# Optimization experiments

Hardware: AMD Instinct MI355X
Metric: run time of the kernel (lower is better)

## Reference

```python
import jax, jax.numpy as jnp
import numpy as np

D_MODEL = 256
D_STATE = 16
D_CONV = 3
D_INNER = 256          # expand=1
D_HALF = D_INNER // 2  # 128
DT_RANK = 16           # ceil(256/16)
B, L0, L1 = 4, 4096, 4096


def setup_inputs() -> dict:
    key = jax.random.key(0)
    ks = jax.random.split(key, 10)
    u_0 = jax.random.normal(ks[0], (B, L0, D_MODEL), jnp.float32)
    u_1 = jax.random.normal(ks[1], (B, L1, D_MODEL), jnp.float32)
    in_proj_w = jax.random.normal(ks[2], (D_INNER, D_MODEL), jnp.float32) * (D_MODEL ** -0.5)
    conv_x_w = jax.random.normal(ks[3], (D_HALF, 1, D_CONV), jnp.float32) * (D_CONV ** -0.5)
    conv_z_w = jax.random.normal(ks[4], (D_HALF, 1, D_CONV), jnp.float32) * (D_CONV ** -0.5)
    x_proj_w = jax.random.normal(ks[5], (DT_RANK + 2 * D_STATE, D_HALF), jnp.float32) * (D_HALF ** -0.5)
    dt_init_std = DT_RANK ** -0.5
    dt_proj_w = jax.random.uniform(ks[6], (D_HALF, DT_RANK), jnp.float32, -dt_init_std, dt_init_std)
    # dt bias = inverse-softplus of dt ~ LogUniform(1e-3, 1e-1)
    dt = jnp.exp(jax.random.uniform(ks[7], (D_HALF,), jnp.float32) * (np.log(0.1) - np.log(0.001)) + np.log(0.001))
    dt = jnp.clip(dt, 1e-4, None)
    dt_proj_b = dt + jnp.log(-jnp.expm1(-dt))
    A_log = jnp.log(jnp.broadcast_to(jnp.arange(1, D_STATE + 1, dtype=jnp.float32), (D_HALF, D_STATE)))
    D_param = jnp.ones((D_HALF,), jnp.float32)
    out_proj_w = jax.random.normal(ks[8], (D_MODEL, D_INNER), jnp.float32) * (D_INNER ** -0.5)
    return {"u_0": u_0, "u_1": u_1, "in_proj_w": in_proj_w, "conv_x_w": conv_x_w,
            "conv_z_w": conv_z_w, "x_proj_w": x_proj_w, "dt_proj_w": dt_proj_w,
            "dt_proj_b": dt_proj_b, "A_log": A_log, "D": D_param, "out_proj_w": out_proj_w}


def _dwconv(x, w):
    # x: [B, C, L], w: [C, 1, K] depthwise, padding='same', no bias (conv_bias//2 == 0)
    return jax.lax.conv_general_dilated(
        x, w, window_strides=(1,), padding='SAME',
        feature_group_count=x.shape[1], dimension_numbers=('NCH', 'OIH', 'NCH'))


def _selective_scan(u, delta, A, Bm, Cm, Dv):
    # u, delta: [B, L, d]; A: [d, n]; Bm, Cm: [B, L, n]; Dv: [d]
    dA = jnp.exp(delta[..., None] * A)                       # [B, L, d, n]
    dBu = (delta * u)[..., None] * Bm[:, :, None, :]         # [B, L, d, n]
    def combine(c1, c2):
        a1, b1 = c1
        a2, b2 = c2
        return a2 * a1, a2 * b1 + b2
    _, h = jax.lax.associative_scan(combine, (dA, dBu), axis=1)  # h: [B, L, d, n]
    return jnp.einsum('bldn,bln->bld', h, Cm) + u * Dv


def _stream(u, in_proj_w, conv_x_w, conv_z_w, x_proj_w, dt_proj_w, dt_proj_b, A, D, out_proj_w):
    xz = jnp.einsum('bld,ed->ble', u, in_proj_w)             # [B, L, d_inner]
    x, z = jnp.split(xz, 2, axis=-1)                         # [B, L, d_half] each
    x = jnp.swapaxes(x, 1, 2)                                # [B, d_half, L]
    z = jnp.swapaxes(z, 1, 2)
    x_f = jax.nn.silu(_dwconv(x, conv_x_w))
    z_f = jax.nn.silu(_dwconv(z, conv_z_w))
    xf = jnp.swapaxes(x_f, 1, 2)                             # [B, L, d_half]
    dbl = jnp.einsum('bld,ed->ble', xf, x_proj_w)            # [B, L, dt_rank + 2n]
    dt, Bm, Cm = jnp.split(dbl, [DT_RANK, DT_RANK + D_STATE], axis=-1)
    dt = jnp.einsum('blr,dr->bld', dt, dt_proj_w)
    delta = jax.nn.softplus(dt + dt_proj_b)                  # delta_bias + delta_softplus
    y = _selective_scan(xf, delta, A, Bm, Cm, D)             # [B, L, d_half]
    cat = jnp.concatenate([y, jnp.swapaxes(z_f, 1, 2)], axis=-1)  # [B, L, d_inner]
    return jnp.einsum('ble,oe->blo', cat, out_proj_w)


def reference(u_0, u_1, in_proj_w, conv_x_w, conv_z_w, x_proj_w, dt_proj_w, dt_proj_b, A_log, D, out_proj_w):
    A = -jnp.exp(A_log)
    out0 = _stream(u_0, in_proj_w, conv_x_w, conv_z_w, x_proj_w, dt_proj_w, dt_proj_b, A, D, out_proj_w)
    out1 = _stream(u_1, in_proj_w, conv_x_w, conv_z_w, x_proj_w, dt_proj_w, dt_proj_b, A, D, out_proj_w)
    return (out0, out1)
```

## Files before the change

kernel.cpp:

```cpp
#include <hip/hip_runtime.h>
#include <hip/hip_bf16.h>
#include <cstdint>

#define DEV __device__ __forceinline__

typedef __attribute__((ext_vector_type(8))) short short8;
typedef __attribute__((ext_vector_type(4))) float f32x4;
typedef __attribute__((ext_vector_type(4))) unsigned short us4;
typedef __attribute__((ext_vector_type(8))) unsigned short us8;

DEV unsigned short f2bf(float x) {
    unsigned int u = __float_as_uint(x);
    unsigned int r = (u + 0x7FFFu + ((u >> 16) & 1u)) >> 16;
    return (unsigned short)r;
}
DEV float bf2f(unsigned short h) { return __uint_as_float(((unsigned int)h) << 16); }

DEV void gld_lds16(const unsigned short* g, unsigned short* l) {
    __builtin_amdgcn_global_load_lds(
        (const __attribute__((address_space(1))) unsigned int*)g,
        (__attribute__((address_space(3))) unsigned int*)l, 16, 0, 0);
}

#define LL 4096
#define DM 256
#define DH 128
#define SB_TOT 8
#define CH1 32
#define NCH 128
#define LOG2E 1.44269504088896f

__global__ __launch_bounds__(256) void prep_kernel(
    const float* __restrict__ u0, const float* __restrict__ u1,
    const float* __restrict__ inw, const float* __restrict__ outw,
    const float* __restrict__ xpw, const float* __restrict__ dtw,
    unsigned short* __restrict__ ubf, unsigned short* __restrict__ wbi,
    unsigned short* __restrict__ wbo, unsigned short* __restrict__ Wb)
{
    int gid = blockIdx.x * 256 + threadIdx.x;
    int i = gid * 4;
    if (i < 4194304) {
        f32x4 v = *(const f32x4*)&u0[i];
        us4 r = { f2bf(v.x), f2bf(v.y), f2bf(v.z), f2bf(v.w) };
        *(us4*)&ubf[i] = r;
    } else if (i < 8388608) {
        int j = i - 4194304;
        f32x4 v = *(const f32x4*)&u1[j];
        us4 r = { f2bf(v.x), f2bf(v.y), f2bf(v.z), f2bf(v.w) };
        *(us4*)&ubf[4194304 + j] = r;
    } else if (i < 8454144) {
        int j = i - 8388608;
        f32x4 v = *(const f32x4*)&inw[j];
        us4 r = { f2bf(v.x), f2bf(v.y), f2bf(v.z), f2bf(v.w) };
        *(us4*)&wbi[j] = r;
    } else if (i < 8519680) {
        int j = i - 8454144;
        f32x4 v = *(const f32x4*)&outw[j];
        us4 r = { f2bf(v.x), f2bf(v.y), f2bf(v.z), f2bf(v.w) };
        *(us4*)&wbo[j] = r;
    } else if (i < 8540160) {
        int j = i - 8519680;
        int n = j >> 7, k0 = j & 127;
        if (n < 128) {
            float a0 = 0.f, a1 = 0.f, a2 = 0.f, a3 = 0.f;
            const float* dw = dtw + n * 16;
            #pragma unroll
            for (int r = 0; r < 16; ++r) {
                float w = dw[r];
                const float* xr = xpw + r * 128 + k0;
                a0 = fmaf(w, xr[0], a0);
                a1 = fmaf(w, xr[1], a1);
                a2 = fmaf(w, xr[2], a2);
                a3 = fmaf(w, xr[3], a3);
            }
            us4 rr = { f2bf(a0), f2bf(a1), f2bf(a2), f2bf(a3) };
            *(us4*)&Wb[n * 128 + k0] = rr;
        } else {
            f32x4 v = *(const f32x4*)&xpw[(n - 112) * 128 + k0];
            us4 rr = { f2bf(v.x), f2bf(v.y), f2bf(v.z), f2bf(v.w) };
            *(us4*)&Wb[n * 128 + k0] = rr;
        }
    }
}

template<int F32OUT>
__global__ __launch_bounds__(256) void gemm_bt(
    const unsigned short* __restrict__ A, const unsigned short* __restrict__ B,
    float* __restrict__ Cf, unsigned short* __restrict__ Cb)
{
    __shared__ __align__(16) unsigned short As[128 * 32];
    __shared__ __align__(16) unsigned short Bs[128 * 32];
    const int t = threadIdx.x;
    const int m0 = blockIdx.x * 128, n0 = blockIdx.y * 128;
    const int lane = t & 63, wv = t >> 6;
    const int wm = (wv & 1) * 64, wn = (wv >> 1) * 64;
    const int lr = lane & 15, lk = (lane >> 4) * 8;
    const int srow = lane >> 2, scol = (lane & 3) * 8;

    f32x4 acc[4][4] = {};
    for (int kt = 0; kt < 8; ++kt) {
        const int k0 = kt * 32;
        #pragma unroll
        for (int h = 0; h < 2; ++h) {
            const int c = wv + h * 4;
            const unsigned short* ga = A + (size_t)(m0 + c * 16 + srow) * 256 + k0 + scol;
            const unsigned short* gb = B + (size_t)(n0 + c * 16 + srow) * 256 + k0 + scol;
            gld_lds16(ga, &As[c * 512]);
            gld_lds16(gb, &Bs[c * 512]);
        }
        __syncthreads();
        short8 av[4], bv[4];
        #pragma unroll
        for (int i = 0; i < 4; ++i) av[i] = *(const short8*)&As[(wm + i * 16 + lr) * 32 + lk];
        #pragma unroll
        for (int i = 0; i < 4; ++i) bv[i] = *(const short8*)&Bs[(wn + i * 16 + lr) * 32 + lk];
        #pragma unroll
        for (int i = 0; i < 4; ++i)
            #pragma unroll
            for (int j = 0; j < 4; ++j)
                acc[i][j] = __builtin_amdgcn_mfma_f32_16x16x32_bf16(av[i], bv[j], acc[i][j], 0, 0, 0);
        __syncthreads();
    }
    #pragma unroll
    for (int i = 0; i < 4; ++i) {
        #pragma unroll
        for (int j = 0; j < 4; ++j) {
            int r0 = m0 + wm + i * 16 + (lane >> 4) * 4;
            int cc = n0 + wn + j * 16 + lr;
            #pragma unroll
            for (int r = 0; r < 4; ++r) {
                float v = acc[i][j][r];
                if (F32OUT) Cf[(size_t)(r0 + r) * 256 + cc] = v;
                else        Cb[(size_t)(r0 + r) * 256 + cc] = f2bf(v);
            }
        }
    }
}

template<int FUSE_SCAN>
__global__ __launch_bounds__(256) void convproj_k(
    const unsigned short* __restrict__ xz, const unsigned short* __restrict__ Wb,
    const float* __restrict__ wx, const float* __restrict__ wz,
    const float* __restrict__ dtb, const float* __restrict__ alog,
    float* __restrict__ xf, unsigned short* __restrict__ catb,
    float* __restrict__ delta, float* __restrict__ BC,
    float* __restrict__ P, float* __restrict__ H)
{
    __shared__ __align__(16) char smem[35840];
    unsigned short* As = (unsigned short*)smem;
    float* dl_s = (float*)smem;
    float* xf_s = (float*)(smem + 16896);
    float* bc_s = (float*)(smem + 33792);
    const int t = threadIdx.x;
    const int kk = blockIdx.x & 7, yy = blockIdx.x >> 3;
    const int m0 = (4 * kk + (yy & 3) + 32 * (yy >> 2)) * 32;

    #pragma unroll
    for (int i = 0; i < 4; ++i) {
        int s = t + i * 256;
        int r = s >> 5, g = s & 31;
        int gr = m0 + r;
        int l = gr & 4095;
        int c; const float* wp; const unsigned short* bp;
        if (g < 16) { c = g * 8;        wp = wx; bp = xz + (size_t)gr * 256 + c; }
        else        { c = (g - 16) * 8; wp = wz; bp = xz + (size_t)gr * 256 + 128 + c; }
        us8 zz = (us8)0;
        us8 vm = (l > 0)    ? *(const us8*)(bp - 256) : zz;
        us8 v0 = *(const us8*)bp;
        us8 vp = (l < 4095) ? *(const us8*)(bp + 256) : zz;
        float o[8];
        #pragma unroll
        for (int j = 0; j < 8; ++j) {
            int cc = c + j;
            float v = bf2f(vm[j]) * wp[cc * 3] + bf2f(v0[j]) * wp[cc * 3 + 1]
                    + bf2f(vp[j]) * wp[cc * 3 + 2];
            v = v / (1.f + __expf(-v));
            o[j] = v;
        }
        us8 rb8 = { f2bf(o[0]), f2bf(o[1]), f2bf(o[2]), f2bf(o[3]),
                    f2bf(o[4]), f2bf(o[5]), f2bf(o[6]), f2bf(o[7]) };
        if (g < 16) {
            *(us8*)&As[r * 136 + c] = rb8;
            *(f32x4*)&xf_s[r * 132 + c]     = *(f32x4*)&o[0];
            *(f32x4*)&xf_s[r * 132 + c + 4] = *(f32x4*)&o[4];
            *(f32x4*)&xf[(size_t)gr * 128 + c]     = *(f32x4*)&o[0];
            *(f32x4*)&xf[(size_t)gr * 128 + c + 4] = *(f32x4*)&o[4];
        } else {
            *(us8*)&catb[(size_t)gr * 256 + 128 + c] = rb8;
        }
    }
    __syncthreads();
    const int lane = t & 63, wv = t >> 6;
    const int lr = lane & 15, lk = (lane >> 4) * 8;
    const int rt = (wv & 1) * 16;
    const int jbase = (wv >> 1) * 5;
    f32x4 acc[5] = {};
    #pragma unroll
    for (int kt = 0; kt < 4; ++kt) {
        const int k0 = kt * 32;
        short8 av = *(const short8*)&As[(rt + lr) * 136 + k0 + lk];
        #pragma unroll
        for (int j = 0; j < 5; ++j) {
            short8 bv = *(const short8*)(Wb + ((jbase + j) * 16 + lr) * 128 + k0 + lk);
            acc[j] = __builtin_amdgcn_mfma_f32_16x16x32_bf16(av, bv, acc[j], 0, 0, 0);
        }
    }
    __syncthreads();
    const int r0 = (lane >> 4) * 4;
    #pragma unroll
    for (int j = 0; j < 5; ++j) {
        int jj = jbase + j;
        int col = jj * 16 + lr;
        #pragma unroll
        for (int r = 0; r < 4; ++r) {
            float v = acc[j][r];
            int lrow = rt + r0 + r;
            size_t row = (size_t)m0 + lrow;
            if (jj < 8) {
                float x = v + dtb[col];
                float sp = (x > 20.f) ? x : __logf(1.f + __expf(x));
                delta[row * 128 + col] = sp;
                if (FUSE_SCAN) dl_s[lrow * 132 + col] = sp;
            } else {
                BC[row * 32 + (col - 128)] = v;
                if (FUSE_SCAN && jj == 8) bc_s[lrow * 16 + lr] = v;
            }
        }
    }
    if (!FUSE_SCAN) return;

    __syncthreads();
    const int hh = t >> 7, tl = t & 127;
    const int sb = m0 >> 12;
    const int ch = (m0 & 4095) >> 5;
    float Ar[8];
    #pragma unroll
    for (int n = 0; n < 8; ++n) Ar[n] = -__expf(alog[tl * 16 + hh * 8 + n]) * LOG2E;
    float h[8], p[8];
    #pragma unroll
    for (int n = 0; n < 8; ++n) { h[n] = 0.f; p[n] = 1.f; }
    #pragma unroll 4
    for (int i = 0; i < CH1; ++i) {
        float dt = dl_s[i * 132 + tl];
        float du = dt * xf_s[i * 132 + tl];
        float bl[8];
        *(f32x4*)&bl[0] = *(const f32x4*)&bc_s[i * 16 + hh * 8];
        *(f32x4*)&bl[4] = *(const f32x4*)&bc_s[i * 16 + hh * 8 + 4];
        #pragma unroll
        for (int n = 0; n < 8; ++n) {
            float a = exp2f(dt * Ar[n]);
            h[n] = fmaf(a, h[n], du * bl[n]);
            p[n] *= a;
        }
    }
    size_t ob = (((size_t)sb * NCH + ch) * 128 + tl) * 16 + hh * 8;
    f32x4 pv0 = { p[0], p[1], p[2], p[3] };
    f32x4 pv1 = { p[4], p[5], p[6], p[7] };
    f32x4 hv0 = { h[0], h[1], h[2], h[3] };
    f32x4 hv1 = { h[4], h[5], h[6], h[7] };
    *(f32x4*)&P[ob]     = pv0;
    *(f32x4*)&P[ob + 4] = pv1;
    *(f32x4*)&H[ob]     = hv0;
    *(f32x4*)&H[ob + 4] = hv1;
}

__global__ __launch_bounds__(128) void scan_p1(
    const float* __restrict__ delta, const float* __restrict__ xf,
    const float* __restrict__ BC, const float* __restrict__ alog,
    float* __restrict__ P, float* __restrict__ H)
{
    __shared__ float b_s[CH1 * 16];
    int t = threadIdx.x;
    int ch = blockIdx.x, sb = blockIdx.y;
    size_t rb = (size_t)sb * LL + (size_t)ch * CH1;
    {
        int row = t >> 2, c4 = (t & 3) * 4;
        *(f32x4*)&b_s[row * 16 + c4] = *(const f32x4*)&BC[(rb + row) * 32 + c4];
    }
    __syncthreads();
    float Ar[16];
    #pragma unroll
    for (int n = 0; n < 16; ++n) Ar[n] = -__expf(alog[t * 16 + n]) * LOG2E;
    float dtr[32], ur[32];
    #pragma unroll
    for (int i = 0; i < 32; ++i) dtr[i] = delta[(rb + i) * DH + t];
    #pragma unroll
    for (int i = 0; i < 32; ++i) ur[i] = xf[(rb + i) * DH + t];
    float h[16], p[16];
    #pragma unroll
    for (int n = 0; n < 16; ++n) { h[n] = 0.f; p[n] = 1.f; }
    for (int i = 0; i < CH1; ++i) {
        float dt = dtr[i];
        float du = dt * ur[i];
        float bl[16];
        *(f32x4*)&bl[0]  = *(const f32x4*)&b_s[i * 16];
        *(f32x4*)&bl[4]  = *(const f32x4*)&b_s[i * 16 + 4];
        *(f32x4*)&bl[8]  = *(const f32x4*)&b_s[i * 16 + 8];
        *(f32x4*)&bl[12] = *(const f32x4*)&b_s[i * 16 + 12];
        #pragma unroll
        for (int n = 0; n < 16; ++n) {
            float a = exp2f(dt * Ar[n]);
            h[n] = fmaf(a, h[n], du * bl[n]);
            p[n] *= a;
        }
    }
    size_t ob = (((size_t)sb * NCH + ch) * 128 + t) * 16;
    #pragma unroll
    for (int n4 = 0; n4 < 16; n4 += 4) {
        f32x4 pv = { p[n4], p[n4 + 1], p[n4 + 2], p[n4 + 3] };
        f32x4 hv = { h[n4], h[n4 + 1], h[n4 + 2], h[n4 + 3] };
        *(f32x4*)&P[ob + n4] = pv;
        *(f32x4*)&H[ob + n4] = hv;
    }
}

__global__ __launch_bounds__(256) void scan_p2(const float* __restrict__ P, float* __restrict__ H)
{
    __shared__ float Ps[NCH * 16], Hs[NCH * 16];
    int t = threadIdx.x;
    int d = blockIdx.x, sb = blockIdx.y;
    for (int q = t; q < NCH * 4; q += 256) {
        int ch = q >> 2, c4 = (q & 3) * 4;
        size_t g = (((size_t)sb * NCH + ch) * 128 + d) * 16 + c4;
        *(f32x4*)&Ps[ch * 16 + c4] = *(const f32x4*)&P[g];
        *(f32x4*)&Hs[ch * 16 + c4] = *(const f32x4*)&H[g];
    }
    __syncthreads();
    if (t < 16) {
        float hin = 0.f;
        for (int c = 0; c < NCH; ++c) {
            float pp = Ps[c * 16 + t], hl = Hs[c * 16 + t];
            Hs[c * 16 + t] = hin;
            hin = fmaf(pp, hin, hl);
        }
    }
    __syncthreads();
    for (int q = t; q < NCH * 4; q += 256) {
        int ch = q >> 2, c4 = (q & 3) * 4;
        size_t g = (((size_t)sb * NCH + ch) * 128 + d) * 16 + c4;
        *(f32x4*)&H[g] = *(const f32x4*)&Hs[ch * 16 + c4];
    }
}

__global__ __launch_bounds__(128) void scan_p3(
    const float* __restrict__ delta, const float* __restrict__ xf,
    const float* __restrict__ BC, const float* __restrict__ alog,
    const float* __restrict__ Dp, const float* __restrict__ H,
    unsigned short* __restrict__ catb)
{
    __shared__ float b_s[CH1 * 16];
    __shared__ float c_s[CH1 * 16];
    int t = threadIdx.x;
    int ch = blockIdx.x, sb = blockIdx.y;
    size_t rb = (size_t)sb * LL + (size_t)ch * CH1;
    {
        int row = t >> 2, c4 = (t & 3) * 4;
        *(f32x4*)&b_s[row * 16 + c4] = *(const f32x4*)&BC[(rb + row) * 32 + c4];
        *(f32x4*)&c_s[row * 16 + c4] = *(const f32x4*)&BC[(rb + row) * 32 + 16 + c4];
    }
    __syncthreads();
    float Ar[16];
    #pragma unroll
    for (int n = 0; n < 16; ++n) Ar[n] = -__expf(alog[t * 16 + n]) * LOG2E;
    float Dv = Dp[t];
    float dtr[32], ur[32];
    #pragma unroll
    for (int i = 0; i < 32; ++i) dtr[i] = delta[(rb + i) * DH + t];
    #pragma unroll
    for (int i = 0; i < 32; ++i) ur[i] = xf[(rb + i) * DH + t];
    size_t ob = (((size_t)sb * NCH + ch) * 128 + t) * 16;
    float h[16];
    #pragma unroll
    for (int n4 = 0; n4 < 16; n4 += 4) {
        f32x4 hv = *(const f32x4*)&H[ob + n4];
        h[n4] = hv.x; h[n4 + 1] = hv.y; h[n4 + 2] = hv.z; h[n4 + 3] = hv.w;
    }
    for (int i = 0; i < CH1; ++i) {
        float dt = dtr[i];
        float uu = ur[i];
        float du = dt * uu;
        float bl[16], cl[16];
        *(f32x4*)&bl[0]  = *(const f32x4*)&b_s[i * 16];
        *(f32x4*)&bl[4]  = *(const f32x4*)&b_s[i * 16 + 4];
        *(f32x4*)&bl[8]  = *(const f32x4*)&b_s[i * 16 + 8];
        *(f32x4*)&bl[12] = *(const f32x4*)&b_s[i * 16 + 12];
        *(f32x4*)&cl[0]  = *(const f32x4*)&c_s[i * 16];
        *(f32x4*)&cl[4]  = *(const f32x4*)&c_s[i * 16 + 4];
        *(f32x4*)&cl[8]  = *(const f32x4*)&c_s[i * 16 + 8];
        *(f32x4*)&cl[12] = *(const f32x4*)&c_s[i * 16 + 12];
        float y0 = uu * Dv, y1 = 0.f, y2 = 0.f, y3 = 0.f;
        #pragma unroll
        for (int n = 0; n < 16; n += 4) {
            float a0 = exp2f(dt * Ar[n]);
            float a1 = exp2f(dt * Ar[n + 1]);
            float a2 = exp2f(dt * Ar[n + 2]);
            float a3 = exp2f(dt * Ar[n + 3]);
            h[n]     = fmaf(a0, h[n],     du * bl[n]);
            h[n + 1] = fmaf(a1, h[n + 1], du * bl[n + 1]);
            h[n + 2] = fmaf(a2, h[n + 2], du * bl[n + 2]);
            h[n + 3] = fmaf(a3, h[n + 3], du * bl[n + 3]);
            y0 = fmaf(h[n],     cl[n],     y0);
            y1 = fmaf(h[n + 1], cl[n + 1], y1);
            y2 = fmaf(h[n + 2], cl[n + 2], y2);
            y3 = fmaf(h[n + 3], cl[n + 3], y3);
        }
        float y = (y0 + y1) + (y2 + y3);
        catb[(rb + i) * DM + t] = f2bf(y);
    }
}

extern "C" void kernel_launch(void* const* d_in, const int* in_sizes, int n_in,
                              void* d_out, int out_size, void* d_ws, size_t ws_size,
                              hipStream_t stream) {
    const float* u0   = (const float*)d_in[0];
    const float* u1   = (const float*)d_in[1];
    const float* inw  = (const float*)d_in[2];
    const float* cxw  = (const float*)d_in[3];
    const float* czw  = (const float*)d_in[4];
    const float* xpw  = (const float*)d_in[5];
    const float* dtw  = (const float*)d_in[6];
    const float* dtb  = (const float*)d_in[7];
    const float* alog = (const float*)d_in[8];
    const float* Dp   = (const float*)d_in[9];
    const float* outw = (const float*)d_in[10];

    char* ws = (char*)d_ws;
    unsigned short* ubf  = (unsigned short*)(ws + 0);
    float* delta         = (float*)(ws + 0);
    unsigned short* xzbf = (unsigned short*)(ws + 16777216);
    float* P_a           = (float*)(ws + 16777216);
    float* H_a           = (float*)(ws + 25165824);
    float* xf            = (float*)(ws + 33554432);
    float* BC            = (float*)(ws + 50331648);
    unsigned short* catb = (unsigned short*)(ws + 54525952);
    unsigned short* wbi  = (unsigned short*)(ws + 71303168);
    unsigned short* wbo  = (unsigned short*)(ws + 71434240);
    unsigned short* Wb   = (unsigned short*)(ws + 71565312);
    float* P_f           = (float*)(ws + 71606272);
    float* H_f           = (float*)(ws + 79994880);

    float* outp = (float*)d_out;

    prep_kernel<<<8340, 256, 0, stream>>>(u0, u1, inw, outw, xpw, dtw, ubf, wbi, wbo, Wb);
    gemm_bt<0><<<dim3(256, 2), 256, 0, stream>>>(ubf, wbi, nullptr, xzbf);

    if (ws_size >= 88383488ull) {
        convproj_k<1><<<1024, 256, 0, stream>>>(xzbf, Wb, cxw, czw, dtb, alog,
                                                xf, catb, delta, BC, P_f, H_f);
        scan_p2<<<dim3(128, 8), 256, 0, stream>>>(P_f, H_f);
        scan_p3<<<dim3(NCH, 8), 128, 0, stream>>>(delta, xf, BC, alog, Dp, H_f, catb);
    } else {
        convproj_k<0><<<1024, 256, 0, stream>>>(xzbf, Wb, cxw, czw, dtb, alog,
                                                xf, catb, delta, BC, nullptr, nullptr);
        scan_p1<<<dim3(NCH, 8), 128, 0, stream>>>(delta, xf, BC, alog, P_a, H_a);
        scan_p2<<<dim3(128, 8), 256, 0, stream>>>(P_a, H_a);
        scan_p3<<<dim3(NCH, 8), 128, 0, stream>>>(delta, xf, BC, alog, Dp, H_a, catb);
    }
    gemm_bt<1><<<dim3(256, 2), 256, 0, stream>>>(catb, wbo, outp, nullptr);
}
```

Baseline: 212.9 us.

## Reorder chunk-state buffers by state quad and hoist conv weights into registers

The P/H chunk-state arrays move from a [chunk][d][16] layout to a [chunk][state-quad][d][4] layout. Consecutive threads now write contiguous 16-byte vectors in the scan kernels, which coalesces their stores and loads, while scan_p2 gathers 16-byte pieces from four strided rows. Separately, the conv/proj kernel now has each thread handle a fixed channel group across rows, so its 24 depthwise weights load once into registers instead of through repeated scalar global loads. Register pressure rises slightly, and scan_p2's reads become more scattered.

```diff
diff --git a/kernel.cpp b/kernel.cpp
--- a/kernel.cpp
+++ b/kernel.cpp
@@ -29,6 +29,7 @@
 #define CH1 32
 #define NCH 128
 #define LOG2E 1.44269504088896f
+
 
 __global__ __launch_bounds__(256) void prep_kernel(
     const float* __restrict__ u0, const float* __restrict__ u1,
@@ -155,15 +156,19 @@
     const int kk = blockIdx.x & 7, yy = blockIdx.x >> 3;
     const int m0 = (4 * kk + (yy & 3) + 32 * (yy >> 2)) * 32;
 
+    const int gg = t & 31;
+    const bool isx = gg < 16;
+    const int c = (isx ? gg : gg - 16) * 8;
+    const float* wp = isx ? wx : wz;
+    float wreg[24];
+    #pragma unroll
+    for (int j = 0; j < 6; ++j) *(f32x4*)&wreg[j * 4] = *(const f32x4*)(wp + c * 3 + j * 4);
     #pragma unroll
     for (int i = 0; i < 4; ++i) {
-        int s = t + i * 256;
-        int r = s >> 5, g = s & 31;
+        int r = (t >> 5) + i * 8;
         int gr = m0 + r;
         int l = gr & 4095;
-        int c; const float* wp; const unsigned short* bp;
-        if (g < 16) { c = g * 8;        wp = wx; bp = xz + (size_t)gr * 256 + c; }
-        else        { c = (g - 16) * 8; wp = wz; bp = xz + (size_t)gr * 256 + 128 + c; }
+        const unsigned short* bp = xz + (size_t)gr * 256 + (isx ? c : 128 + c);
         us8 zz = (us8)0;
         us8 vm = (l > 0)    ? *(const us8*)(bp - 256) : zz;
         us8 v0 = *(const us8*)bp;
@@ -171,15 +176,14 @@
         float o[8];
         #pragma unroll
         for (int j = 0; j < 8; ++j) {
-            int cc = c + j;
-            float v = bf2f(vm[j]) * wp[cc * 3] + bf2f(v0[j]) * wp[cc * 3 + 1]
-                    + bf2f(vp[j]) * wp[cc * 3 + 2];
+            float v = bf2f(vm[j]) * wreg[j * 3] + bf2f(v0[j]) * wreg[j * 3 + 1]
+                    + bf2f(vp[j]) * wreg[j * 3 + 2];
             v = v / (1.f + __expf(-v));
             o[j] = v;
         }
         us8 rb8 = { f2bf(o[0]), f2bf(o[1]), f2bf(o[2]), f2bf(o[3]),
                     f2bf(o[4]), f2bf(o[5]), f2bf(o[6]), f2bf(o[7]) };
-        if (g < 16) {
+        if (isx) {
             *(us8*)&As[r * 136 + c] = rb8;
             *(f32x4*)&xf_s[r * 132 + c]     = *(f32x4*)&o[0];
             *(f32x4*)&xf_s[r * 132 + c + 4] = *(f32x4*)&o[4];
@@ -253,15 +257,15 @@
             p[n] *= a;
         }
     }
-    size_t ob = (((size_t)sb * NCH + ch) * 128 + tl) * 16 + hh * 8;
+    size_t qb = (((size_t)sb * NCH + ch) * 4) * 512 + (size_t)tl * 4;
     f32x4 pv0 = { p[0], p[1], p[2], p[3] };
     f32x4 pv1 = { p[4], p[5], p[6], p[7] };
     f32x4 hv0 = { h[0], h[1], h[2], h[3] };
     f32x4 hv1 = { h[4], h[5], h[6], h[7] };
-    *(f32x4*)&P[ob]     = pv0;
-    *(f32x4*)&P[ob + 4] = pv1;
-    *(f32x4*)&H[ob]     = hv0;
-    *(f32x4*)&H[ob + 4] = hv1;
+    *(f32x4*)&P[qb + (size_t)(2 * hh) * 512]     = pv0;
+    *(f32x4*)&P[qb + (size_t)(2 * hh + 1) * 512] = pv1;
+    *(f32x4*)&H[qb + (size_t)(2 * hh) * 512]     = hv0;
+    *(f32x4*)&H[qb + (size_t)(2 * hh + 1) * 512] = hv1;
 }
 
 __global__ __launch_bounds__(128) void scan_p1(
@@ -304,13 +308,13 @@
             p[n] *= a;
         }
     }
-    size_t ob = (((size_t)sb * NCH + ch) * 128 + t) * 16;
-    #pragma unroll
-    for (int n4 = 0; n4 < 16; n4 += 4) {
-        f32x4 pv = { p[n4], p[n4 + 1], p[n4 + 2], p[n4 + 3] };
-        f32x4 hv = { h[n4], h[n4 + 1], h[n4 + 2], h[n4 + 3] };
-        *(f32x4*)&P[ob + n4] = pv;
-        *(f32x4*)&H[ob + n4] = hv;
+    size_t qb = (((size_t)sb * NCH + ch) * 4) * 512 + (size_t)t * 4;
+    #pragma unroll
+    for (int n4 = 0; n4 < 4; ++n4) {
+        f32x4 pv = { p[n4 * 4], p[n4 * 4 + 1], p[n4 * 4 + 2], p[n4 * 4 + 3] };
+        f32x4 hv = { h[n4 * 4], h[n4 * 4 + 1], h[n4 * 4 + 2], h[n4 * 4 + 3] };
+        *(f32x4*)&P[qb + (size_t)n4 * 512] = pv;
+        *(f32x4*)&H[qb + (size_t)n4 * 512] = hv;
     }
 }
 
@@ -319,11 +323,11 @@
     __shared__ float Ps[NCH * 16], Hs[NCH * 16];
     int t = threadIdx.x;
     int d = blockIdx.x, sb = blockIdx.y;
-    for (int q = t; q < NCH * 4; q += 256) {
-        int ch = q >> 2, c4 = (q & 3) * 4;
-        size_t g = (((size_t)sb * NCH + ch) * 128 + d) * 16 + c4;
-        *(f32x4*)&Ps[ch * 16 + c4] = *(const f32x4*)&P[g];
-        *(f32x4*)&Hs[ch * 16 + c4] = *(const f32x4*)&H[g];
+    for (int q = t; q < 512; q += 256) {
+        int ch = q >> 2, n4 = q & 3;
+        size_t g = (((size_t)sb * NCH + ch) * 4 + n4) * 512 + (size_t)d * 4;
+        *(f32x4*)&Ps[ch * 16 + n4 * 4] = *(const f32x4*)&P[g];
+        *(f32x4*)&Hs[ch * 16 + n4 * 4] = *(const f32x4*)&H[g];
     }
     __syncthreads();
     if (t < 16) {
@@ -335,10 +339,10 @@
         }
     }
     __syncthreads();
-    for (int q = t; q < NCH * 4; q += 256) {
-        int ch = q >> 2, c4 = (q & 3) * 4;
-        size_t g = (((size_t)sb * NCH + ch) * 128 + d) * 16 + c4;
-        *(f32x4*)&H[g] = *(const f32x4*)&Hs[ch * 16 + c4];
+    for (int q = t; q < 512; q += 256) {
+        int ch = q >> 2, n4 = q & 3;
+        size_t g = (((size_t)sb * NCH + ch) * 4 + n4) * 512 + (size_t)d * 4;
+        *(f32x4*)&H[g] = *(const f32x4*)&Hs[ch * 16 + n4 * 4];
     }
 }
 
@@ -368,12 +372,12 @@
     for (int i = 0; i < 32; ++i) dtr[i] = delta[(rb + i) * DH + t];
     #pragma unroll
     for (int i = 0; i < 32; ++i) ur[i] = xf[(rb + i) * DH + t];
-    size_t ob = (((size_t)sb * NCH + ch) * 128 + t) * 16;
+    size_t qb = (((size_t)sb * NCH + ch) * 4) * 512 + (size_t)t * 4;
     float h[16];
     #pragma unroll
-    for (int n4 = 0; n4 < 16; n4 += 4) {
-        f32x4 hv = *(const f32x4*)&H[ob + n4];
-        h[n4] = hv.x; h[n4 + 1] = hv.y; h[n4 + 2] = hv.z; h[n4 + 3] = hv.w;
+    for (int n4 = 0; n4 < 4; ++n4) {
+        f32x4 hv = *(const f32x4*)&H[qb + (size_t)n4 * 512];
+        h[n4 * 4] = hv.x; h[n4 * 4 + 1] = hv.y; h[n4 * 4 + 2] = hv.z; h[n4 * 4 + 3] = hv.w;
     }
     for (int i = 0; i < CH1; ++i) {
         float dt = dtr[i];
```

Result: slower. 228.6 us (+7.4%).
